# Optimization experiments

Measured on AMD Instinct MI355X. Metric: run time of the kernel, lower is better.

## Reference

```python
import jax, jax.numpy as jnp
import numpy as np

OT_GAMMA = 1.0
OT_EPS = 1e-06
OT_ITER = 20
L2_EPS = 1e-12  # F.normalize default eps


def _forward(ft, fs):
    # X = cat(ft, fs): [2n, d]
    X = jnp.concatenate([ft, fs], axis=0)
    # cosine similarity (F.normalize p=2 along dim=1, then X Xn^T)
    Xn = X / jnp.maximum(jnp.linalg.norm(X, axis=1, keepdims=True), L2_EPS)
    C = Xn @ Xn.T  # [2n, 2n]
    n = C.shape[0] // 2
    M = C[:n, n:]  # teacher-student cross block [n, n]
    # zscore_normalize (torch.std is unbiased -> ddof=1)
    M = (M - M.mean()) / jnp.std(M, ddof=1)

    # sinkhorn(1 - M[None], gamma, eps, maxiters), logspace=False, r=c=None
    Mb = (1.0 - M)[None, :, :]  # [1, n, n]
    B, H, W = Mb.shape
    r = 1.0 / H
    c = 1.0 / W
    P0 = jnp.exp(-OT_GAMMA * (Mb - jnp.min(Mb, axis=2, keepdims=True)))

    def step(carry, _):
        P, done = carry
        alpha = P.sum(axis=2, keepdims=True)        # [B, H, 1]
        P1 = P / alpha * r                          # row-normalize
        beta = P1.sum(axis=1, keepdims=True)        # [B, 1, W]
        new_done = done | (jnp.max(jnp.abs(beta - c)) <= OT_EPS)
        # torch breaks AFTER row-normalization when converged
        P2 = jnp.where(new_done, P1, P1 / beta * c)
        P_next = jnp.where(done, P, P2)             # freeze once converged
        return (P_next, new_done), None

    (P, _), _ = jax.lax.scan(step, (P0, jnp.array(False)), None, length=OT_ITER)
    P = P[0]  # squeeze batch -> [n, n]

    # doubly_normalize
    P = P / P.sum(axis=1, keepdims=True)
    P = P / P.sum(axis=0, keepdims=True)

    # torch.norm(A, 2) with no dim flattens -> Frobenius norm
    I = jnp.eye(P.shape[1], dtype=P.dtype)
    loss_ot = jnp.linalg.norm(P - I)
    return loss_ot, P, M


def setup_inputs() -> dict:
    key = jax.random.key(0)
    k1, k2 = jax.random.split(key)
    ft = jax.random.normal(k1, (4096, 1024), dtype=jnp.float32)
    fs = jax.random.normal(k2, (4096, 1024), dtype=jnp.float32)
    return {"ft": ft, "fs": fs}


def reference(ft, fs):
    return _forward(ft, fs)
```

## Files before the change

kernel.cpp:

```cpp
#include <hip/hip_runtime.h>
#include <stdint.h>
#include <math.h>


#define NN 4096
#define DIM 1024
#define OT_ITERS 20
#define OT_EPS_F 1e-6f
#define RC (1.0f/4096.0f)
#define RPB 16
#define SBT 512

typedef __bf16 bf16_t;
typedef _Float16 half_t;
typedef __bf16 bf16x8 __attribute__((ext_vector_type(8)));
typedef _Float16 halfx8 __attribute__((ext_vector_type(8)));
typedef float floatx4 __attribute__((ext_vector_type(4)));

typedef __attribute__((address_space(1))) void gv_t;
typedef __attribute__((address_space(3))) void lv_t;

__device__ __forceinline__ void gld_lds16(const void* g, void* lds_uniform) {
  uint32_t loff = (uint32_t)(uintptr_t)lds_uniform;
  loff = (uint32_t)__builtin_amdgcn_readfirstlane((int)loff);
  __builtin_amdgcn_global_load_lds((gv_t*)(uintptr_t)g, (lv_t*)(uintptr_t)loff, 16, 0, 0);
}

__device__ __forceinline__ void gbar(uint32_t* bar, uint32_t g) {
  __syncthreads();
  if (threadIdx.x == 0) {
    uint32_t* cnt = bar + ((blockIdx.x >> 5) * 64);
    uint32_t* root = bar + 512;
    uint32_t* gen = bar + 576;
    if (__hip_atomic_fetch_add(cnt, 1u, __ATOMIC_RELEASE, __HIP_MEMORY_SCOPE_AGENT) == 31u) {
      __hip_atomic_store(cnt, 0u, __ATOMIC_RELAXED, __HIP_MEMORY_SCOPE_AGENT);
      if (__hip_atomic_fetch_add(root, 1u, __ATOMIC_ACQ_REL, __HIP_MEMORY_SCOPE_AGENT) == 7u) {
        __hip_atomic_store(root, 0u, __ATOMIC_RELAXED, __HIP_MEMORY_SCOPE_AGENT);
        __hip_atomic_store(gen, g, __ATOMIC_RELEASE, __HIP_MEMORY_SCOPE_AGENT);
      }
    }
    while (__hip_atomic_load(gen, __ATOMIC_RELAXED, __HIP_MEMORY_SCOPE_AGENT) < g)
      __builtin_amdgcn_s_sleep(1);
    __builtin_amdgcn_fence(__ATOMIC_ACQUIRE, "agent");
  }
  __syncthreads();
}

__global__ void init_ws(float* scal, uint32_t* bar) {
  int i = blockIdx.x * 256 + threadIdx.x;
  if (i < 8) ((uint32_t*)scal)[i] = 0u;
  if (i < 640) bar[i] = 0u;
}

__global__ __launch_bounds__(256) void norm_rows(const float* __restrict__ X,
                                                 bf16_t* __restrict__ Y) {
  int tid = threadIdx.x;
  int wave = tid >> 6, lane = tid & 63;
  int row = blockIdx.x * 4 + wave;
  const float* xr = X + (size_t)row * DIM;
  float xv[16];
  float ss = 0.f;
#pragma unroll
  for (int k = 0; k < 16; k++) { xv[k] = xr[lane + 64 * k]; ss += xv[k] * xv[k]; }
#pragma unroll
  for (int off = 1; off < 64; off <<= 1) ss += __shfl_xor(ss, off, 64);
  float inv = rsqrtf(ss);
  bf16_t* yr = Y + (size_t)row * DIM;
#pragma unroll
  for (int k = 0; k < 16; k++) yr[lane + 64 * k] = (bf16_t)(xv[k] * inv);
}

__global__ __launch_bounds__(256) void gemm_bt(const bf16_t* __restrict__ A,
                                               const bf16_t* __restrict__ B,
                                               float* __restrict__ C,
                                               float* __restrict__ sumArr,
                                               float* __restrict__ sqArr,
                                               float* __restrict__ rmPart) {
  __shared__ __align__(16) bf16_t As[128 * 32];
  __shared__ __align__(16) bf16_t Bs[128 * 32];
  __shared__ float sred[8];
  int tid = threadIdx.x;
  int wave = tid >> 6, lane = tid & 63;
  int quad = lane >> 4, l16 = lane & 15;
  int bm = blockIdx.y, bn = blockIdx.x;
  int waveM = wave >> 1, waveN = wave & 1;
  floatx4 acc[4][4] = {};

  for (int k0 = 0; k0 < DIM; k0 += 32) {
#pragma unroll
    for (int t = 0; t < 2; t++) {
      int cbase = t * 256 + wave * 64;
      int c = cbase + lane;
      int row = c >> 2, kc = c & 3;
      gld_lds16(A + (size_t)(bm * 128 + row) * DIM + (k0 + kc * 8), (char*)As + (size_t)cbase * 16);
      gld_lds16(B + (size_t)(bn * 128 + row) * DIM + (k0 + kc * 8), (char*)Bs + (size_t)cbase * 16);
    }
    __syncthreads();
    bf16x8 af[4], bfr[4];
#pragma unroll
    for (int mt = 0; mt < 4; mt++)
      af[mt] = *(const bf16x8*)(As + (waveM * 64 + mt * 16 + l16) * 32 + quad * 8);
#pragma unroll
    for (int nt = 0; nt < 4; nt++)
      bfr[nt] = *(const bf16x8*)(Bs + (waveN * 64 + nt * 16 + l16) * 32 + quad * 8);
#pragma unroll
    for (int mt = 0; mt < 4; mt++)
#pragma unroll
      for (int nt = 0; nt < 4; nt++)
        acc[mt][nt] = __builtin_amdgcn_mfma_f32_16x16x32_bf16(af[mt], bfr[nt], acc[mt][nt], 0, 0, 0);
    __syncthreads();
  }

  float lsum = 0.f, lsq = 0.f;
#pragma unroll
  for (int mt = 0; mt < 4; mt++) {
#pragma unroll
    for (int r = 0; r < 4; r++) {
      int gi = bm * 128 + waveM * 64 + mt * 16 + quad * 4 + r;
      float rmax = -3.4e38f;
#pragma unroll
      for (int nt = 0; nt < 4; nt++) {
        float vv = acc[mt][nt][r];
        int gj = bn * 128 + waveN * 64 + nt * 16 + l16;
        C[(size_t)gi * NN + gj] = vv;
        lsum += vv;
        lsq += vv * vv;
        rmax = fmaxf(rmax, vv);
      }
#pragma unroll
      for (int off = 1; off < 16; off <<= 1) rmax = fmaxf(rmax, __shfl_xor(rmax, off, 64));
      if (l16 == 0) rmPart[(size_t)(bn * 2 + waveN) * NN + gi] = rmax;
    }
  }
#pragma unroll
  for (int off = 1; off < 64; off <<= 1) {
    lsum += __shfl_xor(lsum, off, 64);
    lsq += __shfl_xor(lsq, off, 64);
  }
  if (lane == 0) { sred[wave] = lsum; sred[4 + wave] = lsq; }
  __syncthreads();
  if (tid == 0) {
    int bid = bm * 32 + bn;
    sumArr[bid] = sred[0] + sred[1] + sred[2] + sred[3];
    sqArr[bid] = sred[4] + sred[5] + sred[6] + sred[7];
  }
}

__global__ __launch_bounds__(SBT, 1) void sinkhorn_full(
    float* __restrict__ M,
    float* __restrict__ P,
    float* __restrict__ scal,
    const float* __restrict__ sumArr,
    const float* __restrict__ sqArr,
    const float* __restrict__ rmPart,
    float* __restrict__ t,
    float* __restrict__ s,
    float* __restrict__ tg,
    float* __restrict__ devArr,
    uint32_t* __restrict__ bar,
    float* __restrict__ out) {
  __shared__ float red[8 * RPB];
  __shared__ float u_lds[RPB];
  __shared__ float scratch[SBT];
  __shared__ float rowmax_l[RPB];
  __shared__ double dred[16];
  __shared__ float stat_l[2];

  const int b = blockIdx.x;
  const int tid = threadIdx.x;
  const int wave = tid >> 6, lane = tid & 63;
  const int g0 = b * RPB;
  const int c0 = tid * 8;
  uint32_t bg = 0;

  {
    double ds = (double)sumArr[tid] + (double)sumArr[tid + 512];
    double dq = (double)sqArr[tid] + (double)sqArr[tid + 512];
#pragma unroll
    for (int off = 1; off < 64; off <<= 1) {
      ds += __shfl_xor(ds, off, 64);
      dq += __shfl_xor(dq, off, 64);
    }
    if (lane == 0) { dred[wave] = ds; dred[8 + wave] = dq; }
  }
  {
    int row = tid >> 5, half = tid & 31;
    float rm = fmaxf(rmPart[(size_t)(half * 2) * NN + g0 + row],
                     rmPart[(size_t)(half * 2 + 1) * NN + g0 + row]);
#pragma unroll
    for (int off = 1; off < 32; off <<= 1) rm = fmaxf(rm, __shfl_xor(rm, off, 64));
    if (half == 0) rowmax_l[row] = rm;
  }
  __syncthreads();
  if (tid == 0) {
    double sum = 0.0, sumsq = 0.0;
#pragma unroll
    for (int w = 0; w < 8; w++) { sum += dred[w]; sumsq += dred[8 + w]; }
    double Nd = (double)NN * (double)NN;
    double meand = sum / Nd;
    double var = (sumsq - sum * sum / Nd) / (Nd - 1.0);
    stat_l[0] = (float)meand;
    stat_l[1] = (float)(1.0 / sqrt(var));
  }
  __syncthreads();
  const float mean = stat_l[0], istd = stat_l[1];

  halfx8 kreg[RPB];
#pragma unroll
  for (int i = 0; i < RPB; i++) {
    float rmax = rowmax_l[i];
    float* mrow = M + (size_t)(g0 + i) * NN + c0;
    float4 a = *(const float4*)mrow;
    float4 bb = *(const float4*)(mrow + 4);
    float4 sa, sb;
    sa.x = (a.x - mean) * istd;  sa.y = (a.y - mean) * istd;
    sa.z = (a.z - mean) * istd;  sa.w = (a.w - mean) * istd;
    sb.x = (bb.x - mean) * istd; sb.y = (bb.y - mean) * istd;
    sb.z = (bb.z - mean) * istd; sb.w = (bb.w - mean) * istd;
    *(float4*)mrow = sa;
    *(float4*)(mrow + 4) = sb;
    halfx8 kp;
    kp[0] = (half_t)__expf((a.x - rmax) * istd);
    kp[1] = (half_t)__expf((a.y - rmax) * istd);
    kp[2] = (half_t)__expf((a.z - rmax) * istd);
    kp[3] = (half_t)__expf((a.w - rmax) * istd);
    kp[4] = (half_t)__expf((bb.x - rmax) * istd);
    kp[5] = (half_t)__expf((bb.y - rmax) * istd);
    kp[6] = (half_t)__expf((bb.z - rmax) * istd);
    kp[7] = (half_t)__expf((bb.w - rmax) * istd);
    kreg[i] = kp;
  }

  float vr[8];
#pragma unroll
  for (int q = 0; q < 8; q++) vr[q] = 1.0f;

  auto matvec_phase = [&](float scale) {
    float part[RPB];
#pragma unroll
    for (int i = 0; i < RPB; i++) {
      float p = 0.f;
#pragma unroll
      for (int q = 0; q < 8; q++) p += (float)kreg[i][q] * vr[q];
      part[i] = p;
    }
#pragma unroll
    for (int off = 1; off < 64; off <<= 1)
#pragma unroll
      for (int i = 0; i < RPB; i++) part[i] += __shfl_xor(part[i], off, 64);
    if (lane == 0) {
#pragma unroll
      for (int i = 0; i < RPB; i++) red[wave * RPB + i] = part[i];
    }
    __syncthreads();
    if (tid < RPB) {
      float dsum = 0.f;
#pragma unroll
      for (int w = 0; w < 8; w++) dsum += red[w * RPB + tid];
      u_lds[tid] = scale / dsum;
    }
    __syncthreads();
    float ta[8];
#pragma unroll
    for (int q = 0; q < 8; q++) ta[q] = 0.f;
#pragma unroll
    for (int i = 0; i < RPB; i++) {
      float ui = u_lds[i];
#pragma unroll
      for (int q = 0; q < 8; q++) ta[q] += (float)kreg[i][q] * ui;
    }
    float* tgb = tg + (size_t)b * NN;
#pragma unroll
    for (int q = 0; q < 8; q++) tgb[c0 + q] = ta[q];
  };

  auto colreduce = [&]() -> float {
    int jl = tid & 15, seg = tid >> 4;
    int j = g0 + jl;
    float acc = 0.f;
#pragma unroll
    for (int m = 0; m < 8; m++) acc += tg[(size_t)(seg * 8 + m) * NN + j];
    scratch[tid] = acc;
    __syncthreads();
    float tn = 0.f;
    if (tid < RPB) {
#pragma unroll
      for (int k = 0; k < 32; k++) tn += scratch[tid + RPB * k];
    }
    return tn;
  };

  bool frozen = false;
  for (int it = 0; it < OT_ITERS; it++) {
    if (it > 0) {
      float4 t0 = *(const float4*)(t + c0);
      float4 t1 = *(const float4*)(t + c0 + 4);
      vr[0] = RC / t0.x; vr[1] = RC / t0.y; vr[2] = RC / t0.z; vr[3] = RC / t0.w;
      vr[4] = RC / t1.x; vr[5] = RC / t1.y; vr[6] = RC / t1.z; vr[7] = RC / t1.w;
    }
    matvec_phase(RC);
    gbar(bar, ++bg);
    float tn = colreduce();
    if (tid < RPB) {
      int j = g0 + tid;
      float vj = (it == 0) ? 1.0f : (RC / t[j]);
      float dev = fabsf(vj * tn - RC);
      t[j] = tn;
#pragma unroll
      for (int off = 1; off < RPB; off <<= 1) dev = fmaxf(dev, __shfl_xor(dev, off, 64));
      if (tid == 0) devArr[b] = dev;
    }
    gbar(bar, ++bg);
    float x = (tid < 256) ? devArr[tid] : 0.f;
#pragma unroll
    for (int off = 1; off < 64; off <<= 1) x = fmaxf(x, __shfl_xor(x, off, 64));
    if (lane == 0 && wave < 4) scratch[300 + wave] = x;
    __syncthreads();
    float md = fmaxf(fmaxf(scratch[300], scratch[301]), fmaxf(scratch[302], scratch[303]));
    if (md <= OT_EPS_F) { frozen = true; break; }
  }
  if (!frozen) {
#pragma unroll
    for (int q = 0; q < 8; q++) vr[q] = RC / t[c0 + q];
  }

  matvec_phase(1.0f);
  gbar(bar, ++bg);
  float tn = colreduce();
  if (tid < RPB) s[g0 + tid] = tn;
  gbar(bar, ++bg);

  float4 s0 = *(const float4*)(s + c0);
  float4 s1 = *(const float4*)(s + c0 + 4);
  float isv[8] = {1.0f / s0.x, 1.0f / s0.y, 1.0f / s0.z, 1.0f / s0.w,
                  1.0f / s1.x, 1.0f / s1.y, 1.0f / s1.z, 1.0f / s1.w};
  float ls = 0.f;
#pragma unroll
  for (int i = 0; i < RPB; i++) {
    int gi = g0 + i;
    float wi = u_lds[i];
    float* prow = P + (size_t)gi * NN;
#pragma unroll
    for (int q = 0; q < 8; q++) {
      float p = (float)kreg[i][q] * wi * isv[q];
      prow[c0 + q] = p;
      float d = p - ((gi == c0 + q) ? 1.0f : 0.0f);
      ls += d * d;
    }
  }
#pragma unroll
  for (int off = 1; off < 64; off <<= 1) ls += __shfl_xor(ls, off, 64);
  __syncthreads();
  if (lane == 0) red[wave] = ls;
  __syncthreads();
  if (tid == 0) {
    float tot = 0.f;
#pragma unroll
    for (int w = 0; w < 8; w++) tot += red[w];
    atomicAdd(&scal[4], tot);
  }
  gbar(bar, ++bg);
  if (b == 0 && tid == 0) out[0] = sqrtf(scal[4]);
}

extern "C" void kernel_launch(void* const* d_in, const int* in_sizes, int n_in, void* d_out,
                              int out_size, void* d_ws, size_t ws_size, hipStream_t stream) {
  const float* ft = (const float*)d_in[0];
  const float* fs = (const float*)d_in[1];
  float* out = (float*)d_out;

  char* ws = (char*)d_ws;
  bf16_t* A = (bf16_t*)ws;
  bf16_t* B = (bf16_t*)(ws + (8u << 20));
  float* tg = (float*)(ws + (16u << 20));
  float* fbase = (float*)(ws + (24u << 20));
  float* t = fbase;
  float* s = fbase + 4096;
  float* devArr = fbase + 8192;
  float* scal = fbase + 8448;
  uint32_t* bar = (uint32_t*)(fbase + 8704);
  float* sumArr = fbase + 10240;
  float* sqArr = fbase + 11264;
  float* rmPart = fbase + 16384;

  float* P_out = out + 1;
  float* M_out = out + 1 + (size_t)NN * NN;

  init_ws<<<3, 256, 0, stream>>>(scal, bar);
  norm_rows<<<1024, 256, 0, stream>>>(ft, A);
  norm_rows<<<1024, 256, 0, stream>>>(fs, B);
  gemm_bt<<<dim3(32, 32), 256, 0, stream>>>(A, B, M_out, sumArr, sqArr, rmPart);

  sinkhorn_full<<<256, SBT, 0, stream>>>(M_out, P_out, scal, sumArr, sqArr, rmPart, t, s, tg,
                                         devArr, bar, out);
}
```

Before: 373.0 us.

## Replace tg-buffer column reduction with register-resident column tile and shuffle reduce

```diff
diff --git a/kernel.cpp b/kernel.cpp
--- a/kernel.cpp
+++ b/kernel.cpp
@@ -46,17 +46,18 @@
   __syncthreads();
 }
 
-__global__ void init_ws(float* scal, uint32_t* bar) {
-  int i = blockIdx.x * 256 + threadIdx.x;
-  if (i < 8) ((uint32_t*)scal)[i] = 0u;
-  if (i < 640) bar[i] = 0u;
-}
-
-__global__ __launch_bounds__(256) void norm_rows(const float* __restrict__ X,
-                                                 bf16_t* __restrict__ Y) {
+__global__ __launch_bounds__(256) void norm_rows2(const float* __restrict__ ft,
+                                                  const float* __restrict__ fs,
+                                                  bf16_t* __restrict__ A,
+                                                  bf16_t* __restrict__ B,
+                                                  uint32_t* __restrict__ bar) {
+  int gb = blockIdx.x;
+  const float* X = (gb < 1024) ? ft : fs;
+  bf16_t* Y = (gb < 1024) ? A : B;
+  int bb = gb & 1023;
   int tid = threadIdx.x;
   int wave = tid >> 6, lane = tid & 63;
-  int row = blockIdx.x * 4 + wave;
+  int row = bb * 4 + wave;
   const float* xr = X + (size_t)row * DIM;
   float xv[16];
   float ss = 0.f;
@@ -68,6 +69,9 @@
   bf16_t* yr = Y + (size_t)row * DIM;
 #pragma unroll
   for (int k = 0; k < 16; k++) yr[lane + 64 * k] = (bf16_t)(xv[k] * inv);
+  if (gb == 0) {
+    for (int i = tid; i < 640; i += 256) bar[i] = 0u;
+  }
 }
 
 __global__ __launch_bounds__(256) void gemm_bt(const bf16_t* __restrict__ A,
@@ -76,8 +80,8 @@
                                                float* __restrict__ sumArr,
                                                float* __restrict__ sqArr,
                                                float* __restrict__ rmPart) {
-  __shared__ __align__(16) bf16_t As[128 * 32];
-  __shared__ __align__(16) bf16_t Bs[128 * 32];
+  __shared__ __align__(16) bf16_t As[2][128 * 32];
+  __shared__ __align__(16) bf16_t Bs[2][128 * 32];
   __shared__ float sred[8];
   int tid = threadIdx.x;
   int wave = tid >> 6, lane = tid & 63;
@@ -86,29 +90,40 @@
   int waveM = wave >> 1, waveN = wave & 1;
   floatx4 acc[4][4] = {};
 
-  for (int k0 = 0; k0 < DIM; k0 += 32) {
+  auto stage = [&](int k0, int buf) {
 #pragma unroll
     for (int t = 0; t < 2; t++) {
       int cbase = t * 256 + wave * 64;
       int c = cbase + lane;
       int row = c >> 2, kc = c & 3;
-      gld_lds16(A + (size_t)(bm * 128 + row) * DIM + (k0 + kc * 8), (char*)As + (size_t)cbase * 16);
-      gld_lds16(B + (size_t)(bn * 128 + row) * DIM + (k0 + kc * 8), (char*)Bs + (size_t)cbase * 16);
-    }
-    __syncthreads();
+      gld_lds16(A + (size_t)(bm * 128 + row) * DIM + (k0 + kc * 8),
+                (char*)&As[buf][0] + (size_t)cbase * 16);
+      gld_lds16(B + (size_t)(bn * 128 + row) * DIM + (k0 + kc * 8),
+                (char*)&Bs[buf][0] + (size_t)cbase * 16);
+    }
+  };
+
+  stage(0, 0);
+  asm volatile("s_waitcnt vmcnt(0)" ::: "memory");
+  __builtin_amdgcn_s_barrier();
+  int cur = 0;
+  for (int k0 = 0; k0 < DIM; k0 += 32) {
+    if (k0 + 32 < DIM) stage(k0 + 32, cur ^ 1);
     bf16x8 af[4], bfr[4];
 #pragma unroll
     for (int mt = 0; mt < 4; mt++)
-      af[mt] = *(const bf16x8*)(As + (waveM * 64 + mt * 16 + l16) * 32 + quad * 8);
+      af[mt] = *(const bf16x8*)(&As[cur][0] + (waveM * 64 + mt * 16 + l16) * 32 + quad * 8);
 #pragma unroll
     for (int nt = 0; nt < 4; nt++)
-      bfr[nt] = *(const bf16x8*)(Bs + (waveN * 64 + nt * 16 + l16) * 32 + quad * 8);
+      bfr[nt] = *(const bf16x8*)(&Bs[cur][0] + (waveN * 64 + nt * 16 + l16) * 32 + quad * 8);
 #pragma unroll
     for (int mt = 0; mt < 4; mt++)
 #pragma unroll
       for (int nt = 0; nt < 4; nt++)
         acc[mt][nt] = __builtin_amdgcn_mfma_f32_16x16x32_bf16(af[mt], bfr[nt], acc[mt][nt], 0, 0, 0);
-    __syncthreads();
+    asm volatile("s_waitcnt vmcnt(0)" ::: "memory");
+    __builtin_amdgcn_s_barrier();
+    cur ^= 1;
   }
 
   float lsum = 0.f, lsq = 0.f;
@@ -146,88 +161,119 @@
   }
 }
 
-__global__ __launch_bounds__(SBT, 1) void sinkhorn_full(
-    float* __restrict__ M,
-    float* __restrict__ P,
-    float* __restrict__ scal,
-    const float* __restrict__ sumArr,
-    const float* __restrict__ sqArr,
-    const float* __restrict__ rmPart,
+__global__ __launch_bounds__(256) void row_stats(const float* __restrict__ sumArr,
+                                                 const float* __restrict__ sqArr,
+                                                 const float* __restrict__ rmPart,
+                                                 float* __restrict__ rowmax,
+                                                 float* __restrict__ scal) {
+  int tid = threadIdx.x;
+  int row = blockIdx.x * 256 + tid;
+  float rm = -3.4e38f;
+#pragma unroll 8
+  for (int p = 0; p < 64; p++) rm = fmaxf(rm, rmPart[(size_t)p * NN + row]);
+  rowmax[row] = rm;
+  if (blockIdx.x == 0) {
+    double ds = (double)sumArr[tid] + (double)sumArr[tid + 256] +
+                (double)sumArr[tid + 512] + (double)sumArr[tid + 768];
+    double dq = (double)sqArr[tid] + (double)sqArr[tid + 256] +
+                (double)sqArr[tid + 512] + (double)sqArr[tid + 768];
+#pragma unroll
+    for (int off = 1; off < 64; off <<= 1) {
+      ds += __shfl_xor(ds, off, 64);
+      dq += __shfl_xor(dq, off, 64);
+    }
+    __shared__ double dr[8];
+    int wave = tid >> 6, lane = tid & 63;
+    if (lane == 0) { dr[wave] = ds; dr[4 + wave] = dq; }
+    __syncthreads();
+    if (tid == 0) {
+      double sum = dr[0] + dr[1] + dr[2] + dr[3];
+      double sumsq = dr[4] + dr[5] + dr[6] + dr[7];
+      double Nd = (double)NN * (double)NN;
+      double meand = sum / Nd;
+      double var = (sumsq - sum * sum / Nd) / (Nd - 1.0);
+      scal[2] = (float)meand;
+      scal[3] = (float)(1.0 / sqrt(var));
+    }
+  }
+}
+
+__global__ __launch_bounds__(SBT, 2) void sinkhorn_full(
+    float* __restrict__ Mraw,
+    float* __restrict__ Mstd,
+    const float* __restrict__ scal,
+    const float* __restrict__ rowmax,
+    float* __restrict__ u,
     float* __restrict__ t,
     float* __restrict__ s,
-    float* __restrict__ tg,
-    float* __restrict__ devArr,
+    float* __restrict__ lossArr,
     uint32_t* __restrict__ bar,
     float* __restrict__ out) {
   __shared__ float red[8 * RPB];
   __shared__ float u_lds[RPB];
-  __shared__ float scratch[SBT];
   __shared__ float rowmax_l[RPB];
-  __shared__ double dred[16];
-  __shared__ float stat_l[2];
+  __shared__ float mdred[8];
 
   const int b = blockIdx.x;
   const int tid = threadIdx.x;
   const int wave = tid >> 6, lane = tid & 63;
   const int g0 = b * RPB;
   const int c0 = tid * 8;
+  const int r0 = tid * 8;
   uint32_t bg = 0;
-
+  const float mean = scal[2], istd = scal[3];
+
+  halfx8 kcol[16];
   {
-    double ds = (double)sumArr[tid] + (double)sumArr[tid + 512];
-    double dq = (double)sqArr[tid] + (double)sqArr[tid + 512];
-#pragma unroll
-    for (int off = 1; off < 64; off <<= 1) {
-      ds += __shfl_xor(ds, off, 64);
-      dq += __shfl_xor(dq, off, 64);
-    }
-    if (lane == 0) { dred[wave] = ds; dred[8 + wave] = dq; }
-  }
-  {
-    int row = tid >> 5, half = tid & 31;
-    float rm = fmaxf(rmPart[(size_t)(half * 2) * NN + g0 + row],
-                     rmPart[(size_t)(half * 2 + 1) * NN + g0 + row]);
-#pragma unroll
-    for (int off = 1; off < 32; off <<= 1) rm = fmaxf(rm, __shfl_xor(rm, off, 64));
-    if (half == 0) rowmax_l[row] = rm;
-  }
+    float rmx[8];
+    *(float4*)&rmx[0] = *(const float4*)(rowmax + r0);
+    *(float4*)&rmx[4] = *(const float4*)(rowmax + r0 + 4);
+#pragma unroll
+    for (int rl = 0; rl < 8; rl++) {
+      const float* mr = Mraw + (size_t)(r0 + rl) * NN + g0;
+      float v16[16];
+      *(float4*)&v16[0] = *(const float4*)(mr);
+      *(float4*)&v16[4] = *(const float4*)(mr + 4);
+      *(float4*)&v16[8] = *(const float4*)(mr + 8);
+      *(float4*)&v16[12] = *(const float4*)(mr + 12);
+      float rm = rmx[rl];
+      halfx8 lo, hi;
+#pragma unroll
+      for (int q = 0; q < 8; q++) {
+        lo[q] = (half_t)__expf((v16[q] - rm) * istd);
+        hi[q] = (half_t)__expf((v16[8 + q] - rm) * istd);
+      }
+      kcol[rl * 2] = lo;
+      kcol[rl * 2 + 1] = hi;
+    }
+  }
+
+  if (tid < RPB) rowmax_l[tid] = rowmax[g0 + tid];
   __syncthreads();
-  if (tid == 0) {
-    double sum = 0.0, sumsq = 0.0;
-#pragma unroll
-    for (int w = 0; w < 8; w++) { sum += dred[w]; sumsq += dred[8 + w]; }
-    double Nd = (double)NN * (double)NN;
-    double meand = sum / Nd;
-    double var = (sumsq - sum * sum / Nd) / (Nd - 1.0);
-    stat_l[0] = (float)meand;
-    stat_l[1] = (float)(1.0 / sqrt(var));
-  }
-  __syncthreads();
-  const float mean = stat_l[0], istd = stat_l[1];
-
   halfx8 kreg[RPB];
 #pragma unroll
   for (int i = 0; i < RPB; i++) {
-    float rmax = rowmax_l[i];
-    float* mrow = M + (size_t)(g0 + i) * NN + c0;
-    float4 a = *(const float4*)mrow;
-    float4 bb = *(const float4*)(mrow + 4);
+    float rm = rowmax_l[i];
+    const float* mr = Mraw + (size_t)(g0 + i) * NN + c0;
+    float* mo = Mstd + (size_t)(g0 + i) * NN + c0;
+    float4 a = *(const float4*)mr;
+    float4 bb = *(const float4*)(mr + 4);
     float4 sa, sb;
     sa.x = (a.x - mean) * istd;  sa.y = (a.y - mean) * istd;
     sa.z = (a.z - mean) * istd;  sa.w = (a.w - mean) * istd;
     sb.x = (bb.x - mean) * istd; sb.y = (bb.y - mean) * istd;
     sb.z = (bb.z - mean) * istd; sb.w = (bb.w - mean) * istd;
-    *(float4*)mrow = sa;
-    *(float4*)(mrow + 4) = sb;
+    *(float4*)mo = sa;
+    *(float4*)(mo + 4) = sb;
     halfx8 kp;
-    kp[0] = (half_t)__expf((a.x - rmax) * istd);
-    kp[1] = (half_t)__expf((a.y - rmax) * istd);
-    kp[2] = (half_t)__expf((a.z - rmax) * istd);
-    kp[3] = (half_t)__expf((a.w - rmax) * istd);
-    kp[4] = (half_t)__expf((bb.x - rmax) * istd);
-    kp[5] = (half_t)__expf((bb.y - rmax) * istd);
-    kp[6] = (half_t)__expf((bb.z - rmax) * istd);
-    kp[7] = (half_t)__expf((bb.w - rmax) * istd);
+    kp[0] = (half_t)__expf((a.x - rm) * istd);
+    kp[1] = (half_t)__expf((a.y - rm) * istd);
+    kp[2] = (half_t)__expf((a.z - rm) * istd);
+    kp[3] = (half_t)__expf((a.w - rm) * istd);
+    kp[4] = (half_t)__expf((bb.x - rm) * istd);
+    kp[5] = (half_t)__expf((bb.y - rm) * istd);
+    kp[6] = (half_t)__expf((bb.z - rm) * istd);
+    kp[7] = (half_t)__expf((bb.w - rm) * istd);
     kreg[i] = kp;
   }
 
@@ -235,7 +281,7 @@
 #pragma unroll
   for (int q = 0; q < 8; q++) vr[q] = 1.0f;
 
-  auto matvec_phase = [&](float scale) {
+  auto row_phase = [&](float scale, bool toLds) {
     float part[RPB];
 #pragma unroll
     for (int i = 0; i < RPB; i++) {
@@ -257,110 +303,140 @@
       float dsum = 0.f;
 #pragma unroll
       for (int w = 0; w < 8; w++) dsum += red[w * RPB + tid];
-      u_lds[tid] = scale / dsum;
-    }
-    __syncthreads();
-    float ta[8];
-#pragma unroll
-    for (int q = 0; q < 8; q++) ta[q] = 0.f;
-#pragma unroll
-    for (int i = 0; i < RPB; i++) {
-      float ui = u_lds[i];
-#pragma unroll
-      for (int q = 0; q < 8; q++) ta[q] += (float)kreg[i][q] * ui;
-    }
-    float* tgb = tg + (size_t)b * NN;
-#pragma unroll
-    for (int q = 0; q < 8; q++) tgb[c0 + q] = ta[q];
+      float uv = scale / dsum;
+      u[g0 + tid] = uv;
+      if (toLds) u_lds[tid] = uv;
+    }
   };
 
-  auto colreduce = [&]() -> float {
-    int jl = tid & 15, seg = tid >> 4;
-    int j = g0 + jl;
-    float acc = 0.f;
-#pragma unroll
-    for (int m = 0; m < 8; m++) acc += tg[(size_t)(seg * 8 + m) * NN + j];
-    scratch[tid] = acc;
-    __syncthreads();
-    float tn = 0.f;
+  auto col_phase = [&](float* dst) {
+    float u8[8];
+    *(float4*)&u8[0] = *(const float4*)(u + r0);
+    *(float4*)&u8[4] = *(const float4*)(u + r0 + 4);
+    float tp[RPB];
+#pragma unroll
+    for (int j = 0; j < RPB; j++) tp[j] = 0.f;
+#pragma unroll
+    for (int rl = 0; rl < 8; rl++) {
+      float uv = u8[rl];
+#pragma unroll
+      for (int q = 0; q < 8; q++) {
+        tp[q] += (float)kcol[rl * 2][q] * uv;
+        tp[8 + q] += (float)kcol[rl * 2 + 1][q] * uv;
+      }
+    }
+#pragma unroll
+    for (int off = 1; off < 64; off <<= 1)
+#pragma unroll
+      for (int j = 0; j < RPB; j++) tp[j] += __shfl_xor(tp[j], off, 64);
+    if (lane == 0) {
+#pragma unroll
+      for (int j = 0; j < RPB; j++) red[wave * RPB + j] = tp[j];
+    }
+    __syncthreads();
     if (tid < RPB) {
-#pragma unroll
-      for (int k = 0; k < 32; k++) tn += scratch[tid + RPB * k];
-    }
-    return tn;
+      float tv = 0.f;
+#pragma unroll
+      for (int w = 0; w < 8; w++) tv += red[w * RPB + tid];
+      dst[g0 + tid] = tv;
+    }
+  };
+
+  auto mdcheck = [&](float* t8) -> float {
+    *(float4*)&t8[0] = *(const float4*)(t + c0);
+    *(float4*)&t8[4] = *(const float4*)(t + c0 + 4);
+    float dev = 0.f;
+#pragma unroll
+    for (int q = 0; q < 8; q++) dev = fmaxf(dev, fabsf(vr[q] * t8[q] - RC));
+#pragma unroll
+    for (int off = 1; off < 64; off <<= 1) dev = fmaxf(dev, __shfl_xor(dev, off, 64));
+    if (lane == 0) mdred[wave] = dev;
+    __syncthreads();
+    float md = mdred[0];
+#pragma unroll
+    for (int w = 1; w < 8; w++) md = fmaxf(md, mdred[w]);
+    __syncthreads();
+    return md;
   };
 
   bool frozen = false;
   for (int it = 0; it < OT_ITERS; it++) {
     if (it > 0) {
-      float4 t0 = *(const float4*)(t + c0);
-      float4 t1 = *(const float4*)(t + c0 + 4);
-      vr[0] = RC / t0.x; vr[1] = RC / t0.y; vr[2] = RC / t0.z; vr[3] = RC / t0.w;
-      vr[4] = RC / t1.x; vr[5] = RC / t1.y; vr[6] = RC / t1.z; vr[7] = RC / t1.w;
-    }
-    matvec_phase(RC);
+      float t8[8];
+      float md = mdcheck(t8);
+      if (md <= OT_EPS_F) { frozen = true; break; }
+#pragma unroll
+      for (int q = 0; q < 8; q++) vr[q] = RC / t8[q];
+    }
+    row_phase(RC, false);
     gbar(bar, ++bg);
-    float tn = colreduce();
-    if (tid < RPB) {
-      int j = g0 + tid;
-      float vj = (it == 0) ? 1.0f : (RC / t[j]);
-      float dev = fabsf(vj * tn - RC);
-      t[j] = tn;
-#pragma unroll
-      for (int off = 1; off < RPB; off <<= 1) dev = fmaxf(dev, __shfl_xor(dev, off, 64));
-      if (tid == 0) devArr[b] = dev;
-    }
+    col_phase(t);
     gbar(bar, ++bg);
-    float x = (tid < 256) ? devArr[tid] : 0.f;
-#pragma unroll
-    for (int off = 1; off < 64; off <<= 1) x = fmaxf(x, __shfl_xor(x, off, 64));
-    if (lane == 0 && wave < 4) scratch[300 + wave] = x;
-    __syncthreads();
-    float md = fmaxf(fmaxf(scratch[300], scratch[301]), fmaxf(scratch[302], scratch[303]));
-    if (md <= OT_EPS_F) { frozen = true; break; }
   }
   if (!frozen) {
-#pragma unroll
-    for (int q = 0; q < 8; q++) vr[q] = RC / t[c0 + q];
-  }
-
-  matvec_phase(1.0f);
+    float t8[8];
+    float md = mdcheck(t8);
+    if (md > OT_EPS_F) {
+#pragma unroll
+      for (int q = 0; q < 8; q++) vr[q] = RC / t8[q];
+    }
+  }
+
+  row_phase(1.0f, true);
   gbar(bar, ++bg);
-  float tn = colreduce();
-  if (tid < RPB) s[g0 + tid] = tn;
+  col_phase(s);
   gbar(bar, ++bg);
 
-  float4 s0 = *(const float4*)(s + c0);
-  float4 s1 = *(const float4*)(s + c0 + 4);
-  float isv[8] = {1.0f / s0.x, 1.0f / s0.y, 1.0f / s0.z, 1.0f / s0.w,
-                  1.0f / s1.x, 1.0f / s1.y, 1.0f / s1.z, 1.0f / s1.w};
+  float s8[8];
+  *(float4*)&s8[0] = *(const float4*)(s + c0);
+  *(float4*)&s8[4] = *(const float4*)(s + c0 + 4);
+  float isv[8];
+#pragma unroll
+  for (int q = 0; q < 8; q++) isv[q] = 1.0f / s8[q];
   float ls = 0.f;
 #pragma unroll
   for (int i = 0; i < RPB; i++) {
     int gi = g0 + i;
     float wi = u_lds[i];
-    float* prow = P + (size_t)gi * NN;
+    float* prow = Mraw + (size_t)gi * NN + c0;
+    float4 pa, pb;
+    float pv[8];
 #pragma unroll
     for (int q = 0; q < 8; q++) {
       float p = (float)kreg[i][q] * wi * isv[q];
-      prow[c0 + q] = p;
+      pv[q] = p;
       float d = p - ((gi == c0 + q) ? 1.0f : 0.0f);
       ls += d * d;
     }
+    pa.x = pv[0]; pa.y = pv[1]; pa.z = pv[2]; pa.w = pv[3];
+    pb.x = pv[4]; pb.y = pv[5]; pb.z = pv[6]; pb.w = pv[7];
+    *(float4*)prow = pa;
+    *(float4*)(prow + 4) = pb;
   }
 #pragma unroll
   for (int off = 1; off < 64; off <<= 1) ls += __shfl_xor(ls, off, 64);
-  __syncthreads();
   if (lane == 0) red[wave] = ls;
   __syncthreads();
   if (tid == 0) {
     float tot = 0.f;
 #pragma unroll
     for (int w = 0; w < 8; w++) tot += red[w];
-    atomicAdd(&scal[4], tot);
+    lossArr[b] = tot;
   }
   gbar(bar, ++bg);
-  if (b == 0 && tid == 0) out[0] = sqrtf(scal[4]);
+  if (b == 0) {
+    float lv = (tid < 256) ? lossArr[tid] : 0.f;
+#pragma unroll
+    for (int off = 1; off < 64; off <<= 1) lv += __shfl_xor(lv, off, 64);
+    if (lane == 0) mdred[wave] = lv;
+    __syncthreads();
+    if (tid == 0) {
+      float tot = 0.f;
+#pragma unroll
+      for (int w = 0; w < 8; w++) tot += mdred[w];
+      out[0] = sqrtf(tot);
+    }
+  }
 }
 
 extern "C" void kernel_launch(void* const* d_in, const int* in_sizes, int n_in, void* d_out,
@@ -372,25 +448,24 @@
   char* ws = (char*)d_ws;
   bf16_t* A = (bf16_t*)ws;
   bf16_t* B = (bf16_t*)(ws + (8u << 20));
-  float* tg = (float*)(ws + (16u << 20));
-  float* fbase = (float*)(ws + (24u << 20));
-  float* t = fbase;
-  float* s = fbase + 4096;
-  float* devArr = fbase + 8192;
-  float* scal = fbase + 8448;
-  uint32_t* bar = (uint32_t*)(fbase + 8704);
-  float* sumArr = fbase + 10240;
-  float* sqArr = fbase + 11264;
-  float* rmPart = fbase + 16384;
-
-  float* P_out = out + 1;
-  float* M_out = out + 1 + (size_t)NN * NN;
-
-  init_ws<<<3, 256, 0, stream>>>(scal, bar);
-  norm_rows<<<1024, 256, 0, stream>>>(ft, A);
-  norm_rows<<<1024, 256, 0, stream>>>(fs, B);
-  gemm_bt<<<dim3(32, 32), 256, 0, stream>>>(A, B, M_out, sumArr, sqArr, rmPart);
-
-  sinkhorn_full<<<256, SBT, 0, stream>>>(M_out, P_out, scal, sumArr, sqArr, rmPart, t, s, tg,
-                                         devArr, bar, out);
-}
+  float* fbase = (float*)(ws + (16u << 20));
+  float* u = fbase;
+  float* t = fbase + 4096;
+  float* s = fbase + 8192;
+  float* rowmax = fbase + 12288;
+  float* scal = fbase + 16384;
+  float* lossArr = fbase + 16640;
+  uint32_t* bar = (uint32_t*)(fbase + 17408);
+  float* sumArr = fbase + 18432;
+  float* sqArr = fbase + 19456;
+  float* rmPart = fbase + 20480;
+
+  float* P_slot = out + 1;
+  float* M_slot = out + 1 + (size_t)NN * NN;
+
+  norm_rows2<<<2048, 256, 0, stream>>>(ft, fs, A, B, bar);
+  gemm_bt<<<dim3(32, 32), 256, 0, stream>>>(A, B, P_slot, sumArr, sqArr, rmPart);
+  row_stats<<<16, 256, 0, stream>>>(sumArr, sqArr, rmPart, rowmax, scal);
+  sinkhorn_full<<<256, SBT, 0, stream>>>(P_slot, M_slot, scal, rowmax, u, t, s,
+                                         lossArr, bar, out);
+}
```

Result: slower. 411.0 us (+10.2%).
